# Kernel optimization log

Hardware: AMD Instinct MI355X
Metric: run time of the kernel (lower is better)

The kernel has to match this reference:

```python
import jax, jax.numpy as jnp
import numpy as np

D = 256; H = 8; NL = 4; NP = 4; DH = D // H
IMG = 2048; SIDE = 256; NUM_INTERP = 2; PTS = NUM_INTERP + 1
SIDE_LENS = (32, 16, 8, 4)
LEVEL_SHAPES = ((256, 256), (128, 128), (64, 64), (32, 32))
IMG_STARTS = (0, 65536, 81920, 86016)   # level starts in full feature pyramid
VAL_STARTS = (0, 1024, 1280, 1344)      # level starts in cropped pyramid (sum=1360)


def layernorm(x, w, b, eps=1e-5):
    m = x.mean(-1, keepdims=True)
    v = ((x - m) ** 2).mean(-1, keepdims=True)
    return (x - m) * jax.lax.rsqrt(v + eps) * w + b


def pos_encode_2d(x, y, dim=128):
    # DETR-style sinusoidal 2D encoding: 64 dims for y, 64 for x, interleaved sin/cos
    half = dim // 2
    dim_t = 10000.0 ** (2.0 * (jnp.arange(half) // 2) / half)
    def enc(v):
        p = v[..., None] / dim_t
        return jnp.concatenate([jnp.sin(p[..., 0::2])[..., None],
                                jnp.cos(p[..., 1::2])[..., None]], -1).reshape(*v.shape, half)
    return jnp.concatenate([enc(y), enc(x)], -1)


def _forward(mask_flatten, tgt, query_pos, edge_coords, src_flatten, valid_ratios,
             in_proj_w, in_proj_b, out_proj_w, out_proj_b,
             norm1_w, norm1_b, norm2_w, norm2_b, norm3_w, norm3_b,
             lin0_w, lin0_b, lin1_w, lin1_b, lin2_w, lin2_b,
             off_w, off_b, attw_w, attw_b, val_w, val_b, oproj_w, oproj_b):
    E = tgt.shape[1]
    N = E * PTS
    # ---- self attention (dropout = identity, eval mode) ----
    qk = tgt + query_pos
    wq, wk, wv = jnp.split(in_proj_w, 3, 0)
    bq, bk, bv = jnp.split(in_proj_b, 3, 0)
    q = ((qk @ wq.T + bq) * (DH ** -0.5)).reshape(1, E, H, DH)
    k = (qk @ wk.T + bk).reshape(1, E, H, DH)
    v = (tgt @ wv.T + bv).reshape(1, E, H, DH)
    att = jax.nn.softmax(jnp.einsum('behd,bfhd->bhef', q, k), -1)
    sa = jnp.einsum('bhef,bfhd->behd', att, v).reshape(1, E, D) @ out_proj_w.T + out_proj_b
    x = layernorm(tgt + sa, norm2_w, norm2_b)

    # ---- geometry: interp points along edges, crop boxes, segment clipping ----
    a = edge_coords[0, :, :2]
    b = edge_coords[0, :, 2:]
    ts = jnp.arange(PTS, dtype=jnp.float32) / NUM_INTERP
    pts = (a[:, None, :] + ts[None, :, None] * (b - a)[:, None, :]).reshape(N, 2)
    ar = jnp.broadcast_to(a[:, None, :], (E, PTS, 2)).reshape(N, 2)
    br = jnp.broadcast_to(b[:, None, :], (E, PTS, 2)).reshape(N, 2)
    c = jnp.floor(pts).astype(jnp.int32)  # int() truncation, coords > 0
    cx, cy = c[:, 0], c[:, 1]
    minx = jnp.maximum(cx - SIDE // 2, 0)
    minx = jnp.where(minx + SIDE > IMG, IMG - SIDE, minx)
    miny = jnp.maximum(cy - SIDE // 2, 0)
    miny = jnp.where(miny + SIDE > IMG, IMG - SIDE, miny)
    fminx = minx.astype(jnp.float32)
    fminy = miny.astype(jnp.float32)
    d = br - ar
    def axis_clip(p0, d0, lo, hi):
        safe = jnp.where(d0 == 0, 1.0, d0)
        t1 = (lo - p0) / safe
        t2 = (hi - p0) / safe
        tlo = jnp.where(d0 == 0, 0.0, jnp.minimum(t1, t2))
        thi = jnp.where(d0 == 0, 1.0, jnp.maximum(t1, t2))
        return tlo, thi
    tlx, thx = axis_clip(ar[:, 0], d[:, 0], fminx, fminx + SIDE)
    tly, thy = axis_clip(ar[:, 1], d[:, 1], fminy, fminy + SIDE)
    t0 = jnp.maximum(jnp.maximum(tlx, tly), 0.0)
    t1 = jnp.maximum(jnp.minimum(jnp.minimum(thx, thy), 1.0), t0)
    ca = ar + t0[:, None] * d   # clipped segment first endpoint
    cb = ar + t1[:, None] * d   # clipped segment second endpoint
    pos_x = jnp.stack([ca[:, 0], cb[:, 0], cx.astype(jnp.float32)], -1)
    pos_y = jnp.stack([ca[:, 1], cb[:, 1], cy.astype(jnp.float32)], -1)
    pe = pos_encode_2d(pos_x, pos_y).reshape(N, -1)  # [N, 384]

    qfeat = jnp.broadcast_to((x + query_pos)[0][:, None, :], (E, PTS, D)).reshape(N, D)
    nq = jnp.concatenate([qfeat, pe], -1) @ lin0_w.T + lin0_b  # linear0, [N, 256]

    ref = jnp.stack([(cx.astype(jnp.float32) - fminx) / SIDE,
                     (cy.astype(jnp.float32) - fminy) / SIDE], -1)  # [N, 2]
    ref4 = ref[:, None, None, :] * valid_ratios[:, None]  # [N, 1, NL, 2]

    # ---- multi-level feature crops (gather) ----
    srcs, masks = [], []
    for l in range(NL):
        h, w = LEVEL_SHAPES[l]
        s = SIDE_LENS[l]
        ratio = IMG // w
        lx = jnp.round(fminx / ratio).astype(jnp.int32)
        ly = jnp.round(fminy / ratio).astype(jnp.int32)
        rows = ly[:, None] + jnp.arange(s)
        cols = lx[:, None] + jnp.arange(s)
        flat = (rows[:, :, None] * w + cols[:, None, :]).reshape(N, s * s)
        srcs.append(src_flatten[0, IMG_STARTS[l]:IMG_STARTS[l] + h * w][flat])
        masks.append(mask_flatten[0, IMG_STARTS[l]:IMG_STARTS[l] + h * w][flat])
    vsrc = jnp.concatenate(srcs, 1)    # [N, 1360, D]
    vmask = jnp.concatenate(masks, 1)  # [N, 1360]

    # ---- MSDeformAttn cross attention ----
    value = vsrc @ val_w.T + val_b
    value = jnp.where(vmask[..., None], 0.0, value).reshape(N, -1, H, DH)
    off = (nq @ off_w.T + off_b).reshape(N, H, NL, NP, 2)
    aw = jax.nn.softmax((nq @ attw_w.T + attw_b).reshape(N, H, NL * NP), -1).reshape(N, H, NL, NP)
    normalizer = jnp.array([[s, s] for s in SIDE_LENS], jnp.float32)  # (w, h) per crop level
    loc = ref4[:, 0, None, :, None, :] + off / normalizer[None, None, :, None, :]  # [N,H,NL,NP,2]
    n_idx = jnp.arange(N)[:, None, None]
    h_idx = jnp.arange(H)[None, :, None]
    out_acc = jnp.zeros((N, H, DH), jnp.float32)
    for l in range(NL):
        s = SIDE_LENS[l]
        vl = value[:, VAL_STARTS[l]:VAL_STARTS[l] + s * s].reshape(N, s, s, H, DH)
        g = loc[:, :, l]  # [N, H, NP, 2]
        px = g[..., 0] * s - 0.5  # grid_sample align_corners=False
        py = g[..., 1] * s - 0.5
        x0 = jnp.floor(px).astype(jnp.int32)
        y0 = jnp.floor(py).astype(jnp.int32)
        fx = px - x0
        fy = py - y0
        def tap(xi, yi):
            ok = (xi >= 0) & (xi < s) & (yi >= 0) & (yi < s)
            val = vl[n_idx, jnp.clip(yi, 0, s - 1), jnp.clip(xi, 0, s - 1), h_idx]
            return jnp.where(ok[..., None], val, 0.0)
        samp = (tap(x0, y0) * ((1 - fx) * (1 - fy))[..., None]
                + tap(x0 + 1, y0) * (fx * (1 - fy))[..., None]
                + tap(x0, y0 + 1) * ((1 - fx) * fy)[..., None]
                + tap(x0 + 1, y0 + 1) * (fx * fy)[..., None])  # [N,H,NP,DH]
        out_acc = out_acc + (aw[:, :, l, :, None] * samp).sum(2)
    ca_out = out_acc.reshape(N, D) @ oproj_w.T + oproj_b  # [N, D]

    # ---- per-edge mean pooling over interpolation samples ----
    pooled = ca_out.reshape(E, PTS, D).mean(1)[None]
    x = layernorm(x + pooled, norm1_w, norm1_b)
    # ---- FFN ----
    ffn = jax.nn.relu(x @ lin1_w.T + lin1_b) @ lin2_w.T + lin2_b
    return layernorm(x + ffn, norm3_w, norm3_b)


def setup_inputs():
    key = jax.random.key(0)
    ks = jax.random.split(key, 16)
    E = 128
    nrm = lambda k, shape, s=1.0: s * jax.random.normal(k, shape, jnp.float32)
    W = lambda k, o, i: nrm(k, (o, i), 0.02)
    theta = jax.random.uniform(ks[2], (E,), minval=0.0, maxval=2.0 * np.pi)
    start = jax.random.uniform(ks[3], (E, 2), minval=250.0, maxval=1798.0)
    end = start + 200.0 * jnp.stack([jnp.cos(theta), jnp.sin(theta)], -1)  # length 200 -> num_interp=2
    return dict(
        tgt=nrm(ks[0], (1, E, D)),
        query_pos=nrm(ks[1], (1, E, D)),
        edge_coords=jnp.concatenate([start, end], -1)[None],
        src_flatten=nrm(ks[4], (1, 87040, D)),
        mask_flatten=jnp.zeros((1, 87040), bool),
        valid_ratios=jnp.ones((1, 4, 2), jnp.float32),
        in_proj_w=W(ks[5], 3 * D, D), in_proj_b=jnp.zeros(3 * D),
        out_proj_w=W(ks[6], D, D), out_proj_b=jnp.zeros(D),
        norm1_w=jnp.ones(D), norm1_b=jnp.zeros(D),
        norm2_w=jnp.ones(D), norm2_b=jnp.zeros(D),
        norm3_w=jnp.ones(D), norm3_b=jnp.zeros(D),
        lin0_w=W(ks[7], D, 640), lin0_b=jnp.zeros(D),
        lin1_w=W(ks[8], 1024, D), lin1_b=jnp.zeros(1024),
        lin2_w=W(ks[9], D, 1024), lin2_b=jnp.zeros(D),
        off_w=W(ks[10], H * NL * NP * 2, D) * 0.1, off_b=jnp.zeros(H * NL * NP * 2),
        attw_w=W(ks[11], H * NL * NP, D), attw_b=jnp.zeros(H * NL * NP),
        val_w=W(ks[12], D, D), val_b=jnp.zeros(D),
        oproj_w=W(ks[13], D, D), oproj_b=jnp.zeros(D),
    )


def reference(tgt, query_pos, edge_coords, src_flatten, mask_flatten, valid_ratios,
              in_proj_w, in_proj_b, out_proj_w, out_proj_b,
              norm1_w, norm1_b, norm2_w, norm2_b, norm3_w, norm3_b,
              lin0_w, lin0_b, lin1_w, lin1_b, lin2_w, lin2_b,
              off_w, off_b, attw_w, attw_b, val_w, val_b, oproj_w, oproj_b):
    return _forward(mask_flatten, tgt, query_pos, edge_coords, src_flatten, valid_ratios,
                    in_proj_w, in_proj_b, out_proj_w, out_proj_b,
                    norm1_w, norm1_b, norm2_w, norm2_b, norm3_w, norm3_b,
                    lin0_w, lin0_b, lin1_w, lin1_b, lin2_w, lin2_b,
                    off_w, off_b, attw_w, attw_b, val_w, val_b, oproj_w, oproj_b)
```

## Files before the change

kernel.cpp:

```cpp
#include <hip/hip_runtime.h>
#include <math.h>


typedef unsigned int uint;

__device__ __forceinline__ float lo16(uint u) { return __uint_as_float(u << 16); }
__device__ __forceinline__ float hi16(uint u) { return __uint_as_float(u & 0xFFFF0000u); }
__device__ __forceinline__ uint bfr(float x) {
    uint u = __float_as_uint(x);
    return (u + 0x7FFFu + ((u >> 16) & 1u)) >> 16;
}

__device__ __forceinline__ float block_sum256w(float v, float* red) {
    int t = threadIdx.x;
    if (t < 256) red[t] = v;
    __syncthreads();
    for (int st = 128; st > 0; st >>= 1) {
        if (t < st) red[t] += red[t + st];
        __syncthreads();
    }
    float r = red[0]; __syncthreads();
    return r;
}

template <int K, int MI, int MO>
__device__ void gemm_unit(const float* __restrict__ IN, const float* __restrict__ IN2,
                          const float* __restrict__ W, const float* __restrict__ B,
                          float* __restrict__ OUT, int O, int OG, int u, float* smem) {
    constexpr int KC = 128;
    constexpr int LDT = KC + 4;
    float* tile = smem;
    int og = u % OG, rg = u / OG;
    int o0 = og * 8, r0 = rg * 64;
    int t = threadIdx.x;
    int r = t & 63;
    int ol = __builtin_amdgcn_readfirstlane(t >> 6);
    int oa = o0 + ol, ob = o0 + 4 + ol;
    const float* Wa = W + (size_t)oa * K;
    const float* Wb = W + (size_t)ob * K;
    float Ba = B[oa], Bb = B[ob];
    float acca = 0.f, accb = 0.f;
    for (int c = 0; c < K / KC; c++) {
        for (int idx = t; idx < 64 * KC; idx += 256) {
            int rr = idx >> 7, ii = idx & (KC - 1);
            int row = r0 + rr, col = c * KC + ii;
            float v;
            if (MI == 0) {
                v = IN[(size_t)row * K + col];
            } else {
                float tv = IN[row * 256 + col];
                v = (o0 < 512) ? tv + IN2[row * 256 + col] : tv;
            }
            tile[rr * LDT + ii] = v;
        }
        __syncthreads();
        const float4* wa4 = (const float4*)(Wa + c * KC);
        const float4* wb4 = (const float4*)(Wb + c * KC);
        const float4* trow = (const float4*)(tile + r * LDT);
        #pragma unroll
        for (int i4 = 0; i4 < KC / 4; i4++) {
            float4 x4 = trow[i4];
            float4 a4 = wa4[i4];
            float4 b4 = wb4[i4];
            acca += x4.x * a4.x; acca += x4.y * a4.y;
            acca += x4.z * a4.z; acca += x4.w * a4.w;
            accb += x4.x * b4.x; accb += x4.y * b4.y;
            accb += x4.z * b4.z; accb += x4.w * b4.w;
        }
        __syncthreads();
    }
    acca += Ba; accb += Bb;
    if (MO == 2) {
        if (oa < 256) acca *= 0.17677669529663687f;
        if (ob < 256) accb *= 0.17677669529663687f;
    }
    OUT[(size_t)(r0 + r) * O + oa] = acca;
    OUT[(size_t)(r0 + r) * O + ob] = accb;
}

__device__ void transpose_unit(const float* __restrict__ in, float* __restrict__ out,
                               int R, int C, int u, float* smem) {
    int TC = C >> 5;
    int tc = u % TC, tr = u / TC;
    int t = threadIdx.x;
    int lr = t >> 5, lc = t & 31;
    #pragma unroll
    for (int rr = 0; rr < 32; rr += 8)
        smem[(rr + lr) * 33 + lc] = in[(size_t)(tr * 32 + rr + lr) * C + tc * 32 + lc];
    __syncthreads();
    #pragma unroll
    for (int rr = 0; rr < 32; rr += 8)
        out[(size_t)(tc * 32 + rr + lr) * R + tr * 32 + lc] = smem[lc * 33 + rr + lr];
    __syncthreads();
}

__device__ void tpack_unit(const float* __restrict__ in, uint* __restrict__ P,
                           int C, int S, int F, int u, float* smem) {
    int TC = C >> 5;
    int tc = u % TC, tr = u / TC;
    int t = threadIdx.x;
    int lr = t >> 5, lc = t & 31;
    #pragma unroll
    for (int rr = 0; rr < 32; rr += 8)
        smem[(rr + lr) * 33 + lc] = in[(size_t)(tr * 32 + rr + lr) * C + tc * 32 + lc];
    __syncthreads();
    #pragma unroll
    for (int rep = 0; rep < 2; rep++) {
        int idx = rep * 256 + t;
        int c2 = idx >> 5, r = idx & 31;
        uint w0 = bfr(smem[r * 33 + 2 * c2]);
        uint w1 = bfr(smem[r * 33 + 2 * c2 + 1]);
        P[(size_t)(tc * 16 + c2) * S + F + tr * 32 + r] = (w1 << 16) | w0;
    }
    __syncthreads();
}

__global__ __launch_bounds__(256) void k_prep(const float* __restrict__ tgt,
                                              const float* __restrict__ qpos,
                                              const float* __restrict__ ipw,
                                              const float* __restrict__ ipb,
                                              const float* __restrict__ opw,
                                              const float* __restrict__ ojw,
                                              const float* __restrict__ valw,
                                              const float* __restrict__ l1w,
                                              const float* __restrict__ l2w,
                                              const float* __restrict__ l0w,
                                              const float* __restrict__ offw,
                                              const float* __restrict__ aww,
                                              float* __restrict__ qkv,
                                              float* __restrict__ opwT,
                                              float* __restrict__ ojwT,
                                              float* __restrict__ valwT,
                                              uint* __restrict__ Pl1,
                                              uint* __restrict__ Pl2,
                                              uint* __restrict__ Pl0,
                                              uint* __restrict__ Poaw) {
    __shared__ __align__(16) float smem[8448];
    int u = blockIdx.x;
    if (u < 192)       gemm_unit<256, 1, 2>(tgt, qpos, ipw, ipb, qkv, 768, 96, u, smem);
    else if (u < 256)  transpose_unit(opw, opwT, 256, 256, u - 192, smem);
    else if (u < 320)  transpose_unit(ojw, ojwT, 256, 256, u - 256, smem);
    else if (u < 384)  transpose_unit(valw, valwT, 256, 256, u - 320, smem);
    else if (u < 640)  tpack_unit(l1w, Pl1, 256, 1024, 0, u - 384, smem);
    else if (u < 896)  tpack_unit(l2w, Pl2, 1024, 256, 0, u - 640, smem);
    else if (u < 1056) tpack_unit(l0w, Pl0, 640, 256, 0, u - 896, smem);
    else if (u < 1120) tpack_unit(offw, Poaw, 256, 384, 0, u - 1056, smem);
    else               tpack_unit(aww, Poaw, 256, 384, 256, u - 1120, smem);
}

__device__ __forceinline__ void edge_geom(const float* __restrict__ ec, int e, int j,
                                          float* pxs, float* pys,
                                          float& fminx, float& fminy,
                                          float& cxf, float& cyf) {
    float ax = ec[e * 4 + 0], ay = ec[e * 4 + 1];
    float bx = ec[e * 4 + 2], by = ec[e * 4 + 3];
    float dx = bx - ax, dy = by - ay;
    float tj = 0.5f * (float)j;
    float ptx = __fadd_rn(ax, __fmul_rn(tj, dx));
    float pty = __fadd_rn(ay, __fmul_rn(tj, dy));
    cxf = floorf(ptx); cyf = floorf(pty);
    int minx = max((int)cxf - 128, 0); if (minx + 256 > 2048) minx = 2048 - 256;
    int miny = max((int)cyf - 128, 0); if (miny + 256 > 2048) miny = 2048 - 256;
    fminx = (float)minx; fminy = (float)miny;
    float tlx, thx, tly, thy;
    if (dx == 0.f) { tlx = 0.f; thx = 1.f; }
    else { float u1 = (fminx - ax) / dx, u2 = (fminx + 256.f - ax) / dx; tlx = fminf(u1, u2); thx = fmaxf(u1, u2); }
    if (dy == 0.f) { tly = 0.f; thy = 1.f; }
    else { float u1 = (fminy - ay) / dy, u2 = (fminy + 256.f - ay) / dy; tly = fminf(u1, u2); thy = fmaxf(u1, u2); }
    float t0 = fmaxf(fmaxf(tlx, tly), 0.f);
    float t1 = fmaxf(fminf(fminf(thx, thy), 1.f), t0);
    pxs[0] = __fadd_rn(ax, __fmul_rn(t0, dx)); pys[0] = __fadd_rn(ay, __fmul_rn(t0, dy));
    pxs[1] = __fadd_rn(ax, __fmul_rn(t1, dx)); pys[1] = __fadd_rn(ay, __fmul_rn(t1, dy));
    pxs[2] = cxf; pys[2] = cyf;
}

__global__ __launch_bounds__(1024) void k_edge(const float* __restrict__ qkv,
                                               const float* __restrict__ tgt,
                                               const float* __restrict__ qpos,
                                               const float* __restrict__ opwT,
                                               const float* __restrict__ opb,
                                               const float* __restrict__ n2w,
                                               const float* __restrict__ n2b,
                                               const float* __restrict__ ec,
                                               const uint* __restrict__ Pl0,
                                               const float* __restrict__ l0b,
                                               const uint* __restrict__ Poaw,
                                               const float* __restrict__ offb,
                                               const float* __restrict__ awb,
                                               float* __restrict__ x1,
                                               float* __restrict__ offatr,
                                               float* __restrict__ refxy,
                                               int* __restrict__ lxly) {
    int n = blockIdx.x, t = threadIdx.x;
    int e = n / 3, j = n - e * 3;
    __shared__ __align__(16) float SH[14208];
    float* xq   = SH;
    float* sq   = SH + 256;
    float* sS   = SH + 512;
    float* smax = SH + 1536;
    float* ssum = SH + 1544;
    float* srow = SH + 1552;
    float* part = SH + 1808;
    float* red  = SH + 2832;
    float* pe    = SH + 256;
    float* nrow  = SH + 640;
    float* partial = SH + 896;
    uint*  wt    = (uint*)(SH + 1920);
    if (t < 256) sq[t] = qkv[e * 768 + t];
    __syncthreads();
    {
        int h = t >> 7, f = t & 127;
        const float* kf = qkv + f * 768 + 256 + h * 32;
        const float* qh = sq + h * 32;
        float s = 0.f;
        #pragma unroll 8
        for (int d = 0; d < 32; d++) s += qh[d] * kf[d];
        sS[t] = s;
    }
    __syncthreads();
    if (t < 8) {
        float m = -1e30f;
        for (int f = 0; f < 128; f++) m = fmaxf(m, sS[t * 128 + f]);
        smax[t] = m;
    }
    __syncthreads();
    sS[t] = __expf(sS[t] - smax[t >> 7]);
    __syncthreads();
    if (t < 8) {
        float s = 0.f;
        for (int f = 0; f < 128; f++) s += sS[t * 128 + f];
        ssum[t] = 1.f / s;
    }
    __syncthreads();
    {
        int o = t & 255, c = t >> 8, h = o >> 5, d = o & 31;
        float acc = 0.f;
        #pragma unroll 8
        for (int f = c * 32; f < c * 32 + 32; f++)
            acc += sS[h * 128 + f] * qkv[f * 768 + 512 + h * 32 + d];
        part[t] = acc;
    }
    __syncthreads();
    if (t < 256) srow[t] = (part[t] + part[256 + t] + part[512 + t] + part[768 + t]) * ssum[t >> 5];
    __syncthreads();
    {
        int o = t & 255, c = t >> 8;
        float acc = 0.f;
        #pragma unroll 8
        for (int i = c * 64; i < c * 64 + 64; i++) acc += srow[i] * opwT[(size_t)i * 256 + o];
        part[t] = acc;
    }
    __syncthreads();
    {
        float acc = 0.f;
        if (t < 256) acc = part[t] + part[256 + t] + part[512 + t] + part[768 + t] + opb[t] + tgt[e * 256 + t];
        float mean = block_sum256w(acc, red) * (1.f / 256.f);
        float d0 = acc - mean;
        float var = block_sum256w((t < 256) ? d0 * d0 : 0.f, red) * (1.f / 256.f);
        if (t < 256) {
            float xln = d0 * rsqrtf(var + 1e-5f) * n2w[t] + n2b[t];
            if (j == 0) x1[e * 256 + t] = xln;
            xq[t] = xln + qpos[e * 256 + t];
        }
    }
    if (t < 384) {
        float pxs[3], pys[3], fmx, fmy, cxf, cyf;
        edge_geom(ec, e, j, pxs, pys, fmx, fmy, cxf, cyf);
        int jj = t >> 7, tt = t & 127, i = tt & 63, kk = i >> 1;
        float invd = __expf(-(float)kk * (9.210340371976184f / 32.f));
        float vv = (tt < 64) ? pys[jj] : pxs[jj];
        float pp = vv * invd;
        pe[t] = (i & 1) ? __cosf(pp) : __sinf(pp);
    }
    if (t == 0) {
        float pxs[3], pys[3], fmx, fmy, cxf, cyf;
        edge_geom(ec, e, j, pxs, pys, fmx, fmy, cxf, cyf);
        refxy[n * 2 + 0] = (cxf - fmx) * (1.f / 256.f);
        refxy[n * 2 + 1] = (cyf - fmy) * (1.f / 256.f);
        lxly[n * 8 + 0] = (int)rintf(fmx * 0.125f);
        lxly[n * 8 + 1] = (int)rintf(fmx * 0.0625f);
        lxly[n * 8 + 2] = (int)rintf(fmx * 0.03125f);
        lxly[n * 8 + 3] = (int)rintf(fmx * 0.015625f);
        lxly[n * 8 + 4] = (int)rintf(fmy * 0.125f);
        lxly[n * 8 + 5] = (int)rintf(fmy * 0.0625f);
        lxly[n * 8 + 6] = (int)rintf(fmy * 0.03125f);
        lxly[n * 8 + 7] = (int)rintf(fmy * 0.015625f);
    }
    __syncthreads();
    {
        int o = t & 255, kc = t >> 8;
        float acc = 0.f;
        for (int tk = 0; tk < 10; tk++) {
            const uint4* s4 = (const uint4*)(Pl0 + (size_t)tk * 8192);
            uint4* d4 = (uint4*)wt;
            d4[t] = s4[t];
            d4[1024 + t] = s4[1024 + t];
            __syncthreads();
            const float* inb = (tk < 4) ? (xq + tk * 64) : (pe + tk * 64 - 256);
            #pragma unroll
            for (int kk = 0; kk < 8; kk++) {
                uint u = wt[(kc * 8 + kk) * 256 + o];
                acc += inb[(kc * 8 + kk) * 2] * lo16(u);
                acc += inb[(kc * 8 + kk) * 2 + 1] * hi16(u);
            }
            __syncthreads();
        }
        partial[t] = acc;
    }
    __syncthreads();
    if (t < 256) nrow[t] = partial[t] + partial[256 + t] + partial[512 + t] + partial[768 + t] + l0b[t];
    __syncthreads();
    {
        int o = t % 384, kc = t / 384;
        float acc = 0.f;
        for (int tk = 0; tk < 4; tk++) {
            const uint4* s4 = (const uint4*)(Poaw + (size_t)tk * 12288);
            uint4* d4 = (uint4*)wt;
            d4[t] = s4[t];
            d4[1024 + t] = s4[1024 + t];
            d4[2048 + t] = s4[2048 + t];
            __syncthreads();
            if (t < 768) {
                const float* inb = nrow + tk * 64 + kc * 32;
                #pragma unroll
                for (int kk = 0; kk < 16; kk++) {
                    uint u = wt[(kc * 16 + kk) * 384 + o];
                    acc += inb[kk * 2] * lo16(u);
                    acc += inb[kk * 2 + 1] * hi16(u);
                }
            }
            __syncthreads();
        }
        if (t < 768) partial[t] = acc;
    }
    __syncthreads();
    if (t < 384) {
        float b = (t < 256) ? offb[t] : awb[t - 256];
        offatr[(size_t)n * 384 + t] = partial[t] + partial[384 + t] + b;
    }
}

__global__ __launch_bounds__(256) void k_sample(const float* __restrict__ offatr,
                                                const float* __restrict__ refxy,
                                                const float* __restrict__ vr,
                                                const int* __restrict__ lxly,
                                                const float* __restrict__ src,
                                                const unsigned char* __restrict__ mask,
                                                const float* __restrict__ valwT,
                                                const float* __restrict__ valb,
                                                float* __restrict__ ca) {
    int n = blockIdx.x >> 3, h = blockIdx.x & 7, t = threadIdx.x;
    __shared__ float cw[64];
    __shared__ int cg[64];
    __shared__ float agg[256];
    __shared__ float sl[16], sred[2];
    __shared__ float pagg[32 * 8];
    if (t < 16) sl[t] = offatr[n * 384 + 256 + h * 16 + t];
    __syncthreads();
    if (t == 0) {
        float m = -1e30f;
        for (int i = 0; i < 16; i++) m = fmaxf(m, sl[i]);
        float s = 0.f;
        for (int i = 0; i < 16; i++) s += __expf(sl[i] - m);
        sred[0] = m; sred[1] = 1.f / s;
    }
    __syncthreads();
    if (t < 64) {
        int l = t >> 4, pp = (t >> 2) & 3, tap = t & 3;
        int s = 32 >> l;
        int wl = 256 >> l;
        const int img_starts[4] = {0, 65536, 81920, 86016};
        float a = __expf(sl[l * 4 + pp] - sred[0]) * sred[1];
        float slv = (float)s;
        float gx = refxy[n * 2 + 0] * vr[l * 2 + 0] + offatr[n * 384 + h * 32 + l * 8 + pp * 2 + 0] / slv;
        float gy = refxy[n * 2 + 1] * vr[l * 2 + 1] + offatr[n * 384 + h * 32 + l * 8 + pp * 2 + 1] / slv;
        float px = gx * slv - 0.5f, py = gy * slv - 0.5f;
        float x0 = floorf(px), y0 = floorf(py);
        float fx = px - x0, fy = py - y0;
        int xi = (int)x0 + (tap & 1), yi = (int)y0 + (tap >> 1);
        float wtt = ((tap & 1) ? fx : (1.f - fx)) * ((tap >> 1) ? fy : (1.f - fy));
        int g = -1;
        if (xi >= 0 && xi < s && yi >= 0 && yi < s) {
            int col = lxly[n * 8 + l] + xi;
            int row = lxly[n * 8 + 4 + l] + yi;
            g = img_starts[l] + row * wl + col;
            if (mask[g]) g = -1;
        }
        cw[t] = a * wtt;
        cg[t] = g;
    }
    __syncthreads();
    float acc = 0.f, csum = 0.f;
    for (int tp = 0; tp < 64; tp++) {
        int g = cg[tp];
        if (g >= 0) {
            acc += cw[tp] * src[(size_t)g * 256 + t];
            csum += cw[tp];
        }
    }
    agg[t] = acc;
    __syncthreads();
    {
        int o = t & 31, qtr = t >> 5;
        float pv = 0.f;
        #pragma unroll
        for (int i = 0; i < 32; i++) {
            int ii = qtr * 32 + i;
            pv += agg[ii] * valwT[(size_t)ii * 256 + h * 32 + o];
        }
        pagg[o * 8 + qtr] = pv;
    }
    __syncthreads();
    if (t < 32) {
        float o = 0.f;
        for (int qtr = 0; qtr < 8; qtr++) o += pagg[t * 8 + qtr];
        ca[n * 256 + h * 32 + t] = o + csum * valb[h * 32 + t];
    }
}

__global__ __launch_bounds__(1024) void k_tail(const float* __restrict__ ca,
                                               const float* __restrict__ x1,
                                               const float* __restrict__ ojwT,
                                               const float* __restrict__ ojb,
                                               const float* __restrict__ n1w,
                                               const float* __restrict__ n1b,
                                               const uint* __restrict__ Pl1,
                                               const float* __restrict__ l1b,
                                               const uint* __restrict__ Pl2,
                                               const float* __restrict__ l2b,
                                               const float* __restrict__ n3w,
                                               const float* __restrict__ n3b,
                                               float* __restrict__ out) {
    int e = blockIdx.x, t = threadIdx.x;
    __shared__ float row[256], red[256], x2s[256], h1s[1024], part[1024];
    if (t < 256)
        row[t] = (ca[(3 * e) * 256 + t] + ca[(3 * e + 1) * 256 + t] + ca[(3 * e + 2) * 256 + t]) * (1.f / 3.f);
    __syncthreads();
    {
        int o = t & 255, c = t >> 8;
        float acc = 0.f;
        #pragma unroll 8
        for (int i = c * 64; i < c * 64 + 64; i++) acc += row[i] * ojwT[(size_t)i * 256 + o];
        part[t] = acc;
    }
    __syncthreads();
    {
        float acc = 0.f;
        if (t < 256) acc = part[t] + part[256 + t] + part[512 + t] + part[768 + t] + ojb[t] + x1[e * 256 + t];
        float mean = block_sum256w(acc, red) * (1.f / 256.f);
        float d0 = acc - mean;
        float var = block_sum256w((t < 256) ? d0 * d0 : 0.f, red) * (1.f / 256.f);
        if (t < 256) x2s[t] = d0 * rsqrtf(var + 1e-5f) * n1w[t] + n1b[t];
    }
    __syncthreads();
    {
        float acc = l1b[t];
        #pragma unroll 8
        for (int k2 = 0; k2 < 128; k2++) {
            uint u = Pl1[(size_t)k2 * 1024 + t];
            acc += x2s[2 * k2] * lo16(u);
            acc += x2s[2 * k2 + 1] * hi16(u);
        }
        h1s[t] = fmaxf(acc, 0.f);
    }
    __syncthreads();
    {
        int o = t & 255, c = t >> 8;
        float acc = 0.f;
        #pragma unroll 8
        for (int k2 = c * 128; k2 < c * 128 + 128; k2++) {
            uint u = Pl2[(size_t)k2 * 256 + o];
            acc += h1s[2 * k2] * lo16(u);
            acc += h1s[2 * k2 + 1] * hi16(u);
        }
        part[t] = acc;
    }
    __syncthreads();
    {
        float acc = 0.f;
        if (t < 256) acc = part[t] + part[256 + t] + part[512 + t] + part[768 + t] + l2b[t] + x2s[t];
        float mean = block_sum256w(acc, red) * (1.f / 256.f);
        float d0 = acc - mean;
        float var = block_sum256w((t < 256) ? d0 * d0 : 0.f, red) * (1.f / 256.f);
        if (t < 256) out[e * 256 + t] = d0 * rsqrtf(var + 1e-5f) * n3w[t] + n3b[t];
    }
}

extern "C" void kernel_launch(void* const* d_in, const int* in_sizes, int n_in,
                              void* d_out, int out_size, void* d_ws, size_t ws_size,
                              hipStream_t stream) {
    (void)in_sizes; (void)n_in; (void)out_size; (void)ws_size;
    const float* tgt  = (const float*)d_in[0];
    const float* qpos = (const float*)d_in[1];
    const float* ec   = (const float*)d_in[2];
    const float* src  = (const float*)d_in[3];
    const unsigned char* mask = (const unsigned char*)d_in[4];
    const float* vr   = (const float*)d_in[5];
    const float* ipw  = (const float*)d_in[6];
    const float* ipb  = (const float*)d_in[7];
    const float* opw  = (const float*)d_in[8];
    const float* opb  = (const float*)d_in[9];
    const float* n1w  = (const float*)d_in[10];
    const float* n1b  = (const float*)d_in[11];
    const float* n2w  = (const float*)d_in[12];
    const float* n2b  = (const float*)d_in[13];
    const float* n3w  = (const float*)d_in[14];
    const float* n3b  = (const float*)d_in[15];
    const float* l0w  = (const float*)d_in[16];
    const float* l0b  = (const float*)d_in[17];
    const float* l1w  = (const float*)d_in[18];
    const float* l1b  = (const float*)d_in[19];
    const float* l2w  = (const float*)d_in[20];
    const float* l2b  = (const float*)d_in[21];
    const float* offw = (const float*)d_in[22];
    const float* offb = (const float*)d_in[23];
    const float* aww  = (const float*)d_in[24];
    const float* awb  = (const float*)d_in[25];
    const float* valw = (const float*)d_in[26];
    const float* valb = (const float*)d_in[27];
    const float* ojw  = (const float*)d_in[28];
    const float* ojb  = (const float*)d_in[29];

    float* ws     = (float*)d_ws;
    float* qkv    = ws;
    float* x1     = ws + 98304;
    float* offatr = ws + 131072;
    float* ca     = ws + 278528;
    float* refxy  = ws + 376832;
    int*   lxly   = (int*)(ws + 377600);
    float* opwT   = ws + 380672;
    float* ojwT   = ws + 446208;
    float* valwT  = ws + 511744;
    uint*  Pl1    = (uint*)(ws + 577280);
    uint*  Pl2    = (uint*)(ws + 708352);
    uint*  Pl0    = (uint*)(ws + 839424);
    uint*  Poaw   = (uint*)(ws + 921344);

    k_prep<<<1152, 256, 0, stream>>>(tgt, qpos, ipw, ipb, opw, ojw, valw, l1w, l2w,
                                     l0w, offw, aww,
                                     qkv, opwT, ojwT, valwT, Pl1, Pl2, Pl0, Poaw);
    k_edge<<<384, 1024, 0, stream>>>(qkv, tgt, qpos, opwT, opb, n2w, n2b, ec,
                                     Pl0, l0b, Poaw, offb, awb,
                                     x1, offatr, refxy, lxly);
    k_sample<<<3072, 256, 0, stream>>>(offatr, refxy, vr, lxly, src, mask, valwT, valb, ca);
    k_tail<<<128, 1024, 0, stream>>>(ca, x1, ojwT, ojb, n1w, n1b, Pl1, l1b, Pl2, l2b, n3w, n3b, (float*)d_out);
}
```

Baseline: 297.5 us.

## Merge all heads per point in k_sample and deduplicate gathered source rows

```diff
diff --git a/kernel.cpp b/kernel.cpp
--- a/kernel.cpp
+++ b/kernel.cpp
@@ -340,40 +340,50 @@
     }
 }
 
-__global__ __launch_bounds__(256) void k_sample(const float* __restrict__ offatr,
-                                                const float* __restrict__ refxy,
-                                                const float* __restrict__ vr,
-                                                const int* __restrict__ lxly,
-                                                const float* __restrict__ src,
-                                                const unsigned char* __restrict__ mask,
-                                                const float* __restrict__ valwT,
-                                                const float* __restrict__ valb,
-                                                float* __restrict__ ca) {
-    int n = blockIdx.x >> 3, h = blockIdx.x & 7, t = threadIdx.x;
-    __shared__ float cw[64];
-    __shared__ int cg[64];
-    __shared__ float agg[256];
-    __shared__ float sl[16], sred[2];
-    __shared__ float pagg[32 * 8];
-    if (t < 16) sl[t] = offatr[n * 384 + 256 + h * 16 + t];
-    __syncthreads();
-    if (t == 0) {
+__global__ __launch_bounds__(1024) void k_sample(const float* __restrict__ offatr,
+                                                 const float* __restrict__ refxy,
+                                                 const float* __restrict__ vr,
+                                                 const int* __restrict__ lxly,
+                                                 const float* __restrict__ src,
+                                                 const unsigned char* __restrict__ mask,
+                                                 const float* __restrict__ valwT,
+                                                 const float* __restrict__ valb,
+                                                 float* __restrict__ ca) {
+    int n = blockIdx.x, t = threadIdx.x;
+    __shared__ float sl[128];
+    __shared__ float sm[8], sinv[8];
+    __shared__ float sw[512];
+    __shared__ int   sg[512];
+    __shared__ int   lead[512];
+    __shared__ int   rk[512];
+    __shared__ int   ulist[512];
+    __shared__ int   redi[256];
+    __shared__ float uw[512 * 8];
+    __shared__ float agg[8 * 256];
+    __shared__ float pcs[64];
+    __shared__ float pagg[1024];
+
+    if (t < 128) sl[t] = offatr[(size_t)n * 384 + 256 + t];
+    #pragma unroll
+    for (int z = 0; z < 4; z++) uw[z * 1024 + t] = 0.f;
+    __syncthreads();
+    if (t < 8) {
         float m = -1e30f;
-        for (int i = 0; i < 16; i++) m = fmaxf(m, sl[i]);
+        for (int i = 0; i < 16; i++) m = fmaxf(m, sl[t * 16 + i]);
         float s = 0.f;
-        for (int i = 0; i < 16; i++) s += __expf(sl[i] - m);
-        sred[0] = m; sred[1] = 1.f / s;
-    }
-    __syncthreads();
-    if (t < 64) {
-        int l = t >> 4, pp = (t >> 2) & 3, tap = t & 3;
-        int s = 32 >> l;
-        int wl = 256 >> l;
+        for (int i = 0; i < 16; i++) s += __expf(sl[t * 16 + i] - m);
+        sm[t] = m; sinv[t] = 1.f / s;
+    }
+    __syncthreads();
+    if (t < 512) {
+        int h = t >> 6, r = t & 63;
+        int l = r >> 4, pp = (r >> 2) & 3, tap = r & 3;
+        int s = 32 >> l, wl = 256 >> l;
         const int img_starts[4] = {0, 65536, 81920, 86016};
-        float a = __expf(sl[l * 4 + pp] - sred[0]) * sred[1];
+        float a = __expf(sl[h * 16 + l * 4 + pp] - sm[h]) * sinv[h];
         float slv = (float)s;
-        float gx = refxy[n * 2 + 0] * vr[l * 2 + 0] + offatr[n * 384 + h * 32 + l * 8 + pp * 2 + 0] / slv;
-        float gy = refxy[n * 2 + 1] * vr[l * 2 + 1] + offatr[n * 384 + h * 32 + l * 8 + pp * 2 + 1] / slv;
+        float gx = refxy[n * 2 + 0] * vr[l * 2 + 0] + offatr[(size_t)n * 384 + h * 32 + l * 8 + pp * 2 + 0] / slv;
+        float gy = refxy[n * 2 + 1] * vr[l * 2 + 1] + offatr[(size_t)n * 384 + h * 32 + l * 8 + pp * 2 + 1] / slv;
         float px = gx * slv - 0.5f, py = gy * slv - 0.5f;
         float x0 = floorf(px), y0 = floorf(py);
         float fx = px - x0, fy = py - y0;
@@ -386,35 +396,73 @@
             g = img_starts[l] + row * wl + col;
             if (mask[g]) g = -1;
         }
-        cw[t] = a * wtt;
-        cg[t] = g;
-    }
-    __syncthreads();
-    float acc = 0.f, csum = 0.f;
-    for (int tp = 0; tp < 64; tp++) {
-        int g = cg[tp];
+        sw[t] = a * wtt;
+        sg[t] = g;
+    }
+    __syncthreads();
+    int fi = -1;
+    if (t < 512) {
+        int g = sg[t];
         if (g >= 0) {
-            acc += cw[tp] * src[(size_t)g * 256 + t];
-            csum += cw[tp];
-        }
-    }
-    agg[t] = acc;
-    __syncthreads();
-    {
-        int o = t & 31, qtr = t >> 5;
+            fi = t;
+            for (int jj = 0; jj < t; jj++) if (sg[jj] == g) { fi = jj; break; }
+        }
+        lead[t] = (fi == t) ? 1 : 0;
+    }
+    __syncthreads();
+    if (t < 512 && fi == t) {
+        int r = 0;
+        for (int jj = 0; jj < t; jj++) r += lead[jj];
+        rk[t] = r;
+        ulist[r] = sg[t];
+    }
+    if (t < 256) redi[t] = lead[t] + lead[t + 256];
+    __syncthreads();
+    for (int st = 128; st > 0; st >>= 1) {
+        if (t < st) redi[t] += redi[t + st];
+        __syncthreads();
+    }
+    if (t < 512 && fi >= 0) {
+        int h = t >> 6;
+        atomicAdd(&uw[rk[fi] * 8 + h], sw[t]);
+    }
+    __syncthreads();
+    int U = redi[0];
+    {
+        int ch = t & 255, q = t >> 8;
+        float a0 = 0.f, a1 = 0.f;
+        for (int u = 0; u < U; u++) {
+            int g = ulist[u];
+            float v = src[(size_t)g * 256 + ch];
+            a0 += uw[u * 8 + 2 * q] * v;
+            a1 += uw[u * 8 + 2 * q + 1] * v;
+        }
+        agg[(2 * q) * 256 + ch] = a0;
+        agg[(2 * q + 1) * 256 + ch] = a1;
+    }
+    if (t < 64) {
+        int h = t >> 3, p = t & 7;
+        float s = 0.f;
+        for (int u = p; u < U; u += 8) s += uw[u * 8 + h];
+        pcs[t] = s;
+    }
+    __syncthreads();
+    {
+        int h = t >> 7, rem = t & 127, o = rem & 31, kc = rem >> 5;
+        const float* ag = agg + h * 256 + kc * 64;
+        const float* w = valwT + (size_t)(kc * 64) * 256 + h * 32 + o;
         float pv = 0.f;
-        #pragma unroll
-        for (int i = 0; i < 32; i++) {
-            int ii = qtr * 32 + i;
-            pv += agg[ii] * valwT[(size_t)ii * 256 + h * 32 + o];
-        }
-        pagg[o * 8 + qtr] = pv;
-    }
-    __syncthreads();
-    if (t < 32) {
-        float o = 0.f;
-        for (int qtr = 0; qtr < 8; qtr++) o += pagg[t * 8 + qtr];
-        ca[n * 256 + h * 32 + t] = o + csum * valb[h * 32 + t];
+        #pragma unroll 8
+        for (int i = 0; i < 64; i++) pv += ag[i] * w[(size_t)i * 256];
+        pagg[t] = pv;
+    }
+    __syncthreads();
+    if (t < 256) {
+        int h = t >> 5, o = t & 31;
+        float cs = pcs[h * 8 + 0] + pcs[h * 8 + 1] + pcs[h * 8 + 2] + pcs[h * 8 + 3]
+                 + pcs[h * 8 + 4] + pcs[h * 8 + 5] + pcs[h * 8 + 6] + pcs[h * 8 + 7];
+        float r = pagg[h * 128 + o] + pagg[h * 128 + 32 + o] + pagg[h * 128 + 64 + o] + pagg[h * 128 + 96 + o];
+        ca[(size_t)n * 256 + h * 32 + o] = r + cs * valb[h * 32 + o];
     }
 }
 
@@ -542,6 +590,6 @@
     k_edge<<<384, 1024, 0, stream>>>(qkv, tgt, qpos, opwT, opb, n2w, n2b, ec,
                                      Pl0, l0b, Poaw, offb, awb,
                                      x1, offatr, refxy, lxly);
-    k_sample<<<3072, 256, 0, stream>>>(offatr, refxy, vr, lxly, src, mask, valwT, valb, ca);
+    k_sample<<<384, 1024, 0, stream>>>(offatr, refxy, vr, lxly, src, mask, valwT, valb, ca);
     k_tail<<<128, 1024, 0, stream>>>(ca, x1, ojwT, ojb, n1w, n1b, Pl1, l1b, Pl2, l2b, n3w, n3b, (float*)d_out);
 }
```

Result: faster. 277.2 us (-6.8%).
